# Kernel tuning notes

Hardware: AMD Instinct MI355X
Metric: run time of the kernel (lower is better)

## Reference

```python
import jax, jax.numpy as jnp
import numpy as np

B, T, D = 4, 1024, 512
H, TD = 4, 5
DH = D // H          # per-head value dim
DFF = D // 2         # Clifford FFN half-width
DR = D               # reservoir size
M = 64               # 2**mem_depth leaves
OFFSETS = (-3, -2, -1, 0)  # causal sheaf window=3
EPS = 1e-5

def _ln(x, g, b):
    m = jnp.mean(x, axis=-1, keepdims=True)
    v = jnp.mean((x - m) ** 2, axis=-1, keepdims=True)
    return (x - m) / jnp.sqrt(v + EPS) * g + b

def setup_inputs() -> dict:
    keys = iter(jax.random.split(jax.random.key(0), 64))
    def rn(shape, s=0.02):
        return (jax.random.normal(next(keys), shape) * s).astype(jnp.float32)
    x = jax.random.normal(next(keys), (B, T, D), dtype=jnp.float32)
    # sparse reservoir recurrence matrix (sparsity=0.9)
    wres_mask = (jax.random.uniform(next(keys), (DR, DR)) > 0.9).astype(jnp.float32)
    res_Wres = jax.random.normal(next(keys), (DR, DR)) * wres_mask * 0.05
    eye = jnp.eye(D, dtype=jnp.float32)
    sheaf_Rw = jnp.stack([eye + rn((D, D), 0.01) for _ in OFFSETS])  # [4,D,D]
    return dict(
        x=x,
        ln1_g=jnp.ones((D,)), ln1_b=jnp.zeros((D,)),
        ln2_g=jnp.ones((D,)), ln2_b=jnp.zeros((D,)),
        ln3_g=jnp.ones((D,)), ln3_b=jnp.zeros((D,)),
        ln4_g=jnp.ones((D,)), ln4_b=jnp.zeros((D,)),
        attn_Wp=rn((H * TD, D)), attn_bp=jnp.zeros((H * TD,)),
        attn_Wv=rn((D, D)), attn_Wo=rn((D, D)),
        ffn_Wr=rn((DFF, D)), ffn_br=jnp.zeros((DFF,)),
        ffn_Wi=rn((DFF, D)), ffn_bi=jnp.zeros((DFF,)),
        ffn_Wg=rn((D, D)), ffn_bg=jnp.zeros((D,)),
        ffn_Wout=rn((D, D)), ffn_bout=jnp.zeros((D,)),
        res_Win=rn((DR, D)), res_Wres=res_Wres,
        res_logrho=jnp.float32(0.0), res_leak=jnp.float32(0.3),
        res_readout=rn((D, DR)),
        res_v0=jax.random.normal(next(keys), (DR,), dtype=jnp.float32),
        mem_keys=rn((M, D)), mem_vals=rn((M, D)),
        mem_Wq=rn((D, D)), mem_Wout=rn((D, D)), mem_bout=jnp.zeros((D,)),
        sheaf_Rw=sheaf_Rw, sheaf_Rb=jnp.zeros((len(OFFSETS), D)),
        sheaf_alpha=jnp.float32(0.15),
    )

def reference(x, ln1_g, ln1_b, ln2_g, ln2_b, ln3_g, ln3_b, ln4_g, ln4_b,
              attn_Wp, attn_bp, attn_Wv, attn_Wo,
              ffn_Wr, ffn_br, ffn_Wi, ffn_bi, ffn_Wg, ffn_bg, ffn_Wout, ffn_bout,
              res_Win, res_Wres, res_logrho, res_leak, res_readout, res_v0,
              mem_keys, mem_vals, mem_Wq, mem_Wout, mem_bout,
              sheaf_Rw, sheaf_Rb, sheaf_alpha):
    Bx, Tx, d = x.shape

    def attn_fn(h):  # PAdicAttention, causal
        paths = jax.nn.sigmoid(h @ attn_Wp.T + attn_bp)
        paths = paths.reshape(Bx, Tx, H, TD).transpose(0, 2, 1, 3)   # [B,H,T,TD]
        pq = paths[:, :, :, None, :]
        pk = paths[:, :, None, :, :]
        agree = pq * pk + (1.0 - pq) * (1.0 - pk)                    # [B,H,T,T,TD]
        sim = jnp.sum(jnp.cumprod(agree, axis=-1), axis=-1) / TD     # [B,H,T,T]
        mask = jnp.triu(jnp.ones((Tx, Tx), bool), 1)
        sim = jnp.where(mask[None, None], -jnp.inf, sim)
        a = jax.nn.softmax(sim, axis=-1)
        V = (h @ attn_Wv.T).reshape(Bx, Tx, H, DH).transpose(0, 2, 1, 3)
        ctx = jnp.einsum('bhqk,bhkd->bhqd', a, V)
        return ctx.transpose(0, 2, 1, 3).reshape(Bx, Tx, d) @ attn_Wo.T

    def res_fn(h):  # EchoStateReservoir
        rho_t = jax.nn.sigmoid(res_logrho) * 1.5
        Wd = jax.lax.stop_gradient(res_Wres)
        def pi(v, _):
            v = Wd @ v
            n = jnp.linalg.norm(v)
            return jnp.where(n > 0, v / n, v), None
        v, _ = jax.lax.scan(pi, res_v0, None, length=3)
        rho_c = jax.lax.stop_gradient(jnp.linalg.norm(Wd @ v))
        Ws = res_Wres * (rho_t / jnp.maximum(rho_c, 1e-6))
        lk = jax.nn.sigmoid(res_leak)
        u = h @ res_Win.T                                            # [B,T,dr]
        def step(hs, ut):
            hs = (1.0 - lk) * hs + lk * jnp.tanh(hs @ Ws.T + ut)
            return hs, hs
        _, Hs = jax.lax.scan(step, jnp.zeros((Bx, DR), x.dtype), u.transpose(1, 0, 2))
        return Hs.transpose(1, 0, 2) @ res_readout.T

    def mem_fn(h):  # PAdicMemory
        q = h @ mem_Wq.T
        w = jax.nn.softmax(q @ mem_keys.T / jnp.sqrt(jnp.float32(d)), axis=-1)
        return (w @ mem_vals) @ mem_Wout.T + mem_bout

    def ffn_fn(h):  # CliffordFFN
        r = h @ ffn_Wr.T + ffn_br
        i = h @ ffn_Wi.T + ffn_bi
        prod = jnp.concatenate([r * r - i * i, 2.0 * r * i], axis=-1)
        gate = jax.nn.sigmoid(h @ ffn_Wg.T + ffn_bg)
        return (prod * gate) @ ffn_Wout.T + ffn_bout

    def sheaf_fn(h):  # SheafDiffusion, causal offsets
        lap = jnp.zeros_like(h)
        for idx, delta in enumerate(OFFSETS):
            Rx = h @ sheaf_Rw[idx].T + sheaf_Rb[idx]
            if delta == 0:
                x_nb = h
            else:
                ad = -delta
                x_nb = jnp.concatenate(
                    [jnp.zeros((Bx, ad, d), h.dtype), h[:, :Tx - ad, :]], axis=1)
            lap = lap + (Rx - x_nb) @ sheaf_Rw[idx]   # note: @ W, not W.T (as in source)
        return h - jnp.abs(sheaf_alpha) * lap

    x = x + attn_fn(_ln(x, ln1_g, ln1_b))
    x = x + res_fn(_ln(x, ln2_g, ln2_b))
    x = x + mem_fn(_ln(x, ln3_g, ln3_b))
    x = x + ffn_fn(_ln(x, ln4_g, ln4_b))
    return sheaf_fn(x)
```

## Files before the change

### kernel.cpp

```cpp
#include <hip/hip_runtime.h>
#include <hip/hip_bf16.h>
#include <stdint.h>

typedef unsigned short u16;
typedef unsigned int u32;
typedef unsigned long long u64;
typedef __bf16 bf16x8 __attribute__((ext_vector_type(8)));
typedef float f32x4 __attribute__((ext_vector_type(4)));
typedef int i32x4 __attribute__((ext_vector_type(4)));

__device__ __forceinline__ u16 f2bf(float f){
  unsigned u = __float_as_uint(f);
  u += 0x7fffu + ((u>>16)&1u);
  return (u16)(u>>16);
}
__device__ __forceinline__ float bf2f(u16 h){ return __uint_as_float((u32)h<<16); }
__device__ __forceinline__ float sigm(float x){ return 1.f/(1.f+__expf(-x)); }
__device__ __forceinline__ float tanh_fast(float x){ float e = __expf(2.f*x); return 1.f - 2.f/(e+1.f); }

__device__ __forceinline__ void gl_lds16(const void* g, void* l){
  __builtin_amdgcn_global_load_lds((const __attribute__((address_space(1))) void*)g,
                                   (__attribute__((address_space(3))) void*)l, 16, 0, 0);
}


__global__ __launch_bounds__(128) void prep_weights(
  const float* Wp, const float* Wv, const float* Wo, const float* Win, const float* rd,
  const float* Wq, const float* keys, const float* vals, const float* mWo,
  const float* Wr, const float* Wi, const float* Wg, const float* fWo, const float* Rw,
  const float* bp, const float* fbr, const float* fbi, const float* fbg,
  u16* WpB, u16* WvB, u16* WoB, u16* WinB, u16* rdB,
  u16* WqB, u16* keysB, u16* valsB, u16* mWoB,
  u16* WrB, u16* WiB, u16* WgB, u16* fWoB, u16* RwB,
  float* bpp, float* bpc, float* ss)
{
  int blk = blockIdx.x, t = threadIdx.x;
  if(blk==6912){ if(t<128) bpp[t] = (t<20)? bp[t] : 0.f; return; }
  if(blk==6913){
    for(int j=t; j<1024; j+=128)
      bpc[j] = (j<256)? fbr[j] : (j<512)? fbi[j-256] : fbg[j-512];
    return;
  }
  if(blk==6914){ if(t==0) ss[0]=1.f; else if(t<5) ss[t]=0.f; return; }
  const float* src = nullptr; u16* dst = nullptr; int r;
  bool perm = false;
  if(blk<128){ r=blk; dst=WpB+(size_t)r*512; if(r<20) src=Wp+(size_t)r*512; }
  else if(blk<640){ r=blk-128; dst=WvB+(size_t)r*512; src=Wv+(size_t)r*512; }
  else if(blk<1152){ r=blk-640; dst=WoB+(size_t)r*512; src=Wo+(size_t)r*512; }
  else if(blk<1664){ r=blk-1152; dst=WinB+(size_t)r*512; src=Win+(size_t)r*512; }
  else if(blk<2176){ r=blk-1664; dst=rdB+(size_t)r*512; src=rd+(size_t)r*512; perm=true; }
  else if(blk<2688){ r=blk-2176; dst=WqB+(size_t)r*512; src=Wq+(size_t)r*512; }
  else if(blk<2752){ r=blk-2688; dst=keysB+(size_t)r*512; src=keys+(size_t)r*512; }
  else if(blk<2816){ r=blk-2752; dst=valsB+(size_t)r*512; src=vals+(size_t)r*512; }
  else if(blk<3328){ r=blk-2816; dst=mWoB+(size_t)r*512; src=mWo+(size_t)r*512; }
  else if(blk<3584){ r=blk-3328; dst=WrB+(size_t)r*512; src=Wr+(size_t)r*512; }
  else if(blk<3840){ r=blk-3584; dst=WiB+(size_t)r*512; src=Wi+(size_t)r*512; }
  else if(blk<4352){ r=blk-3840; dst=WgB+(size_t)r*512; src=Wg+(size_t)r*512; }
  else if(blk<4864){ r=blk-4352; dst=fWoB+(size_t)r*512; src=fWo+(size_t)r*512; }
  else { r=blk-4864; dst=RwB+(size_t)r*512; src=Rw+(size_t)r*512; }
  if(src){
    float4 a = *(const float4*)&src[t*4];
    ushort4 o; o.x=f2bf(a.x); o.y=f2bf(a.y); o.z=f2bf(a.z); o.w=f2bf(a.w);
    if(perm){
      int k0 = t*4;
      int base = (k0 & ~63) | ((k0&15)<<2) | ((k0>>4)&3);
      dst[base] = o.x; dst[base+4] = o.y; dst[base+8] = o.z; dst[base+12] = o.w;
    } else {
      *(ushort4*)&dst[t*4] = o;
    }
  } else {
    ushort4 z; z.x=0; z.y=0; z.z=0; z.w=0;
    *(ushort4*)&dst[t*4] = z;
  }
}

__global__ __launch_bounds__(256) void transpose_rw(const float* __restrict__ Rw, u16* __restrict__ RwT){
  __shared__ float tl[32][33];
  int z = blockIdx.z, it = blockIdx.x, jt = blockIdx.y;
  const float* src = Rw + (size_t)z*262144;
  int r = threadIdx.x>>3, c4 = (threadIdx.x&7)*4;
  float4 v = *(const float4*)&src[(size_t)(jt*32+r)*512 + it*32 + c4];
  tl[r][c4+0]=v.x; tl[r][c4+1]=v.y; tl[r][c4+2]=v.z; tl[r][c4+3]=v.w;
  __syncthreads();
  ushort4 o;
  o.x = f2bf(tl[c4+0][r]); o.y = f2bf(tl[c4+1][r]);
  o.z = f2bf(tl[c4+2][r]); o.w = f2bf(tl[c4+3][r]);
  *(ushort4*)&RwT[(size_t)(it*32+r)*2048 + z*512 + jt*32 + c4] = o;
}

__global__ __launch_bounds__(64) void ln_kernel(const float* __restrict__ x, const float* __restrict__ g,
      const float* __restrict__ b, u16* __restrict__ out)
{
  int row = blockIdx.x, lane = threadIdx.x;
  const float* xr = x + (size_t)row*512;
  float4 v0 = *(const float4*)&xr[lane*4];
  float4 v1 = *(const float4*)&xr[256+lane*4];
  float s = v0.x+v0.y+v0.z+v0.w + v1.x+v1.y+v1.z+v1.w;
  float q = v0.x*v0.x+v0.y*v0.y+v0.z*v0.z+v0.w*v0.w + v1.x*v1.x+v1.y*v1.y+v1.z*v1.z+v1.w*v1.w;
  #pragma unroll
  for(int m=1;m<64;m<<=1){ s += __shfl_xor(s,m); q += __shfl_xor(q,m); }
  float mean = s*(1.f/512.f);
  float var  = q*(1.f/512.f) - mean*mean;
  float rstd = rsqrtf(var + 1e-5f);
  float4 g0 = *(const float4*)&g[lane*4], g1 = *(const float4*)&g[256+lane*4];
  float4 b0 = *(const float4*)&b[lane*4], b1 = *(const float4*)&b[256+lane*4];
  ushort4 o0, o1;
  o0.x = f2bf((v0.x-mean)*rstd*g0.x + b0.x); o0.y = f2bf((v0.y-mean)*rstd*g0.y + b0.y);
  o0.z = f2bf((v0.z-mean)*rstd*g0.z + b0.z); o0.w = f2bf((v0.w-mean)*rstd*g0.w + b0.w);
  o1.x = f2bf((v1.x-mean)*rstd*g1.x + b1.x); o1.y = f2bf((v1.y-mean)*rstd*g1.y + b1.y);
  o1.z = f2bf((v1.z-mean)*rstd*g1.z + b1.z); o1.w = f2bf((v1.w-mean)*rstd*g1.w + b1.w);
  *(ushort4*)&out[(size_t)row*512 + lane*4] = o0;
  *(ushort4*)&out[(size_t)row*512 + 256 + lane*4] = o1;
}

template<int EPI>
__global__ __launch_bounds__(256,2) void gemm_nt(
  const u16* __restrict__ A, const u16* __restrict__ Bw, int K, int ldc,
  float* __restrict__ outf, u16* __restrict__ outb,
  const float* __restrict__ bias, const float* __restrict__ resid,
  const float* __restrict__ aux, float* __restrict__ outf2,
  const float* __restrict__ scal, int shift_ad)
{
  __shared__ u16 Al[128*64];
  __shared__ u16 Bl[64*64];
  const int t = threadIdx.x;
  const int bm = blockIdx.x, bn = blockIdx.y;
  const int wid = t>>6, lane = t&63;
  const int wr = wid>>1, wc = wid&1;
  const int fr = lane&15, fq = lane>>4;
  f32x4 acc[4][2] = {};
  const int nK = K>>6;
  const u16* Ab = A + (size_t)(bm*128)*K;
  const u16* Bb = Bw + (size_t)(bn*64)*K;
  const int srow8 = t>>3;
  const int scol = (t&7)*8;
  char* AlB = (char*)Al; char* BlB = (char*)Bl;
  const int lbase = wid*1024;
  for(int bk=0; bk<nK; ++bk){
    #pragma unroll
    for(int c=0;c<4;++c)
      gl_lds16(&Ab[(size_t)(c*32+srow8)*K + bk*64 + scol], AlB + c*4096 + lbase);
    #pragma unroll
    for(int c=0;c<2;++c)
      gl_lds16(&Bb[(size_t)(c*32+srow8)*K + bk*64 + scol], BlB + c*4096 + lbase);
    __syncthreads();
    #pragma unroll
    for(int kk=0;kk<2;++kk){
      bf16x8 af[4], bf[2];
      #pragma unroll
      for(int m=0;m<4;++m) af[m] = *(const bf16x8*)&Al[(wr*64+m*16+fr)*64 + kk*32 + fq*8];
      #pragma unroll
      for(int n=0;n<2;++n) bf[n] = *(const bf16x8*)&Bl[(wc*32+n*16+fr)*64 + kk*32 + fq*8];
      #pragma unroll
      for(int m=0;m<4;++m)
        #pragma unroll
        for(int n=0;n<2;++n)
          acc[m][n] = __builtin_amdgcn_mfma_f32_16x16x32_bf16(af[m], bf[n], acc[m][n], 0,0,0);
    }
    __syncthreads();
  }
  float alpha = 0.f;
  if(EPI==8) alpha = fabsf(scal[0]);
  #pragma unroll
  for(int m=0;m<4;++m){
    int gr0 = bm*128 + wr*64 + m*16 + fq*4;
    #pragma unroll
    for(int n=0;n<2;++n){
      int gc = bn*64 + wc*32 + n*16 + fr;
      float bv = 0.f;
      if(EPI==2||EPI==3||EPI==5||EPI==6||EPI==9||EPI==12) bv = bias[gc];
      if(EPI==10 && gc<128) bv = bias[gc];
      #pragma unroll
      for(int i=0;i<4;++i){
        int r = gr0 + i;
        float v = acc[m][n][i] + bv;
        if(EPI==3) v = sigm(v);
        if(EPI==1||EPI==5||EPI==6) v += resid[(size_t)r*ldc + gc];
        if(EPI==8){
          outf[(size_t)r*ldc + gc] -= alpha*v;
        } else if(EPI==9){
          if(gc<512) outf[(size_t)r*512 + gc] = v;
          else       outf2[(size_t)r*512 + gc-512] = sigm(v);
        } else if(EPI==10){
          if(gc<128) outf[(size_t)r*128 + gc] = sigm(v);
          else       outf2[(size_t)r*512 + gc-128] = v;
        } else if(EPI==11){
          int pc = (gc & ~63) | ((gc&15)<<2) | ((gc>>4)&3);
          outf[(size_t)r*512 + pc] = v;
        } else if(EPI==12){
          int idx = gc>>9;
          int ad = 3 - idx;
          int ts = r & 1023;
          float xnb = 0.f;
          if(ts >= ad) xnb = bf2f(((const u16*)aux)[(size_t)(r-ad)*512 + (gc&511)]);
          outb[(size_t)r*2048 + gc] = f2bf(v - xnb);
        } else {
          if(EPI==0||EPI==1||EPI==2||EPI==3||EPI==5) outf[(size_t)r*ldc + gc] = v;
          if(EPI==6) outf2[(size_t)r*ldc + gc] = v;
          if(EPI==4||EPI==6) outb[(size_t)r*ldc + gc] = f2bf(v);
        }
      }
    }
  }
}

__global__ __launch_bounds__(128) void attn_kernel(
  const float* __restrict__ paths, const float* __restrict__ Vbuf, u16* __restrict__ ctxb)
{
  const int t = threadIdx.x;
  const int qt = blockIdx.x, bh = blockIdx.y;
  const int b = bh>>2, h = bh&3;
  const int rb = b<<10;
  const int ql = t>>2, sub = t&3;
  const int q = qt*32 + ql;
  const int wid = t>>6, lane = t&63;
  const int fr = lane&15, fq = lane>>4;
  __shared__ u16 Vl[128][72];
  __shared__ u16 Pl[32][72];
  __shared__ float pkl[64][6];
  __shared__ float scl[32];
  __shared__ float lsm[32];
  float al[5], bl[5];
  #pragma unroll
  for(int l=0;l<5;++l){
    float p = paths[(size_t)(rb+q)*128 + h*5 + l];
    al[l] = 2.f*p - 1.f; bl[l] = 1.f - p;
  }
  float m_run = -1e30f, l_run = 0.f;
  f32x4 acc[2][4] = {};
  const int nkt = (qt>>1) + 1;
  for(int kt=0; kt<nkt; ++kt){
    int k0 = kt*64;
    for(int i=t; i<320; i+=128){
      int k = i/5, l = i%5;
      pkl[k][l] = paths[(size_t)(rb+k0+k)*128 + h*5 + l];
    }
    {
      int dg = (t&31)*4, kbase = t>>5;
      #pragma unroll
      for(int i=0;i<16;++i){
        int k = kbase + i*4;
        float4 v4 = *(const float4*)&Vbuf[(size_t)(rb+k0+k)*512 + h*128 + dg];
        Vl[dg+0][k] = f2bf(v4.x); Vl[dg+1][k] = f2bf(v4.y);
        Vl[dg+2][k] = f2bf(v4.z); Vl[dg+3][k] = f2bf(v4.w);
      }
    }
    __syncthreads();
    float pj[16]; float tm = -1e30f;
    #pragma unroll
    for(int j=0;j<16;++j){
      int kidx = sub*16 + j;
      int k = k0 + kidx;
      float s;
      if(k <= q){
        float c = al[0]*pkl[kidx][0] + bl[0];
        float sa = c;
        #pragma unroll
        for(int l=1;l<5;++l){ c *= al[l]*pkl[kidx][l] + bl[l]; sa += c; }
        s = sa*0.2f;
      } else s = -1e30f;
      pj[j] = s; tm = fmaxf(tm, s);
    }
    tm = fmaxf(tm, __shfl_xor(tm,1,4));
    tm = fmaxf(tm, __shfl_xor(tm,2,4));
    float m_new = fmaxf(m_run, tm);
    float corr = __expf(m_run - m_new);
    float ls = 0.f;
    #pragma unroll
    for(int j=0;j<16;++j){
      float p = (pj[j] > -1e29f) ? __expf(pj[j]-m_new) : 0.f;
      ls += p;
      Pl[ql][sub*16+j] = f2bf(p);
    }
    l_run = l_run*corr + ls;
    m_run = m_new;
    if(sub==0) scl[ql] = corr;
    __syncthreads();
    #pragma unroll
    for(int m=0;m<2;++m){
      float c0 = scl[m*16+fq*4+0], c1 = scl[m*16+fq*4+1];
      float c2 = scl[m*16+fq*4+2], c3 = scl[m*16+fq*4+3];
      #pragma unroll
      for(int n=0;n<4;++n){ acc[m][n][0]*=c0; acc[m][n][1]*=c1; acc[m][n][2]*=c2; acc[m][n][3]*=c3; }
    }
    #pragma unroll
    for(int kk=0;kk<2;++kk){
      bf16x8 af[2], bf[4];
      #pragma unroll
      for(int m=0;m<2;++m) af[m] = *(const bf16x8*)&Pl[m*16+fr][kk*32+fq*8];
      #pragma unroll
      for(int n=0;n<4;++n) bf[n] = *(const bf16x8*)&Vl[wid*64+n*16+fr][kk*32+fq*8];
      #pragma unroll
      for(int m=0;m<2;++m)
        #pragma unroll
        for(int n=0;n<4;++n)
          acc[m][n] = __builtin_amdgcn_mfma_f32_16x16x32_bf16(af[m], bf[n], acc[m][n], 0,0,0);
    }
    __syncthreads();
  }
  {
    float lt = l_run + __shfl_xor(l_run,1,4);
    lt += __shfl_xor(lt,2,4);
    if(sub==0) lsm[ql] = lt;
  }
  __syncthreads();
  #pragma unroll
  for(int m=0;m<2;++m){
    float inv[4];
    #pragma unroll
    for(int i=0;i<4;++i) inv[i] = 1.f/lsm[m*16+fq*4+i];
    #pragma unroll
    for(int n=0;n<4;++n){
      int row = rb + qt*32 + m*16 + fq*4;
      int col = h*128 + wid*64 + n*16 + fr;
      #pragma unroll
      for(int i=0;i<4;++i)
        ctxb[(size_t)(row+i)*512 + col] = f2bf(acc[m][n][i]*inv[i]);
    }
  }
}

__global__ __launch_bounds__(256) void pmv(const float* __restrict__ W, const float* __restrict__ vin,
                    const float* __restrict__ ssin, float* __restrict__ vout, float* __restrict__ ssout)
{
  __shared__ float vs[512];
  int t = threadIdx.x;
  int j = blockIdx.x*16 + (t>>4), ks = t&15;
  float s = ssin[0];
  float inv = (s>0.f)? rsqrtf(s) : 1.f;
  vs[t] = vin[t]*inv; vs[t+256] = vin[t+256]*inv;
  __syncthreads();
  float p = 0.f;
  const float* wr = &W[(size_t)j*512 + ks*32];
  #pragma unroll
  for(int kk=0;kk<32;++kk) p += wr[kk]*vs[ks*32+kk];
  p += __shfl_xor(p,1,16); p += __shfl_xor(p,2,16); p += __shfl_xor(p,4,16); p += __shfl_xor(p,8,16);
  if(ks==0){ vout[j] = p; atomicAdd(ssout, p*p); }
}

__global__ __launch_bounds__(128) void scale_ws(const float* __restrict__ Wres, const float* __restrict__ ss4,
                         const float* __restrict__ logrho, signed char* __restrict__ WsQ,
                         float* __restrict__ wscale)
{
  __shared__ float wmax[2];
  int j = blockIdx.x, t = threadIdx.x;
  int fr = t&15, blk = t>>4;
  float rho_t = 1.5f * sigm(logrho[0]);
  float rho_c = sqrtf(ss4[0]);
  float sc = rho_t / fmaxf(rho_c, 1e-6f);
  float w[4];
  #pragma unroll
  for(int cg=0;cg<4;++cg) w[cg] = Wres[(size_t)j*512 + blk*64 + cg*16 + fr]*sc;
  float m = fmaxf(fmaxf(fabsf(w[0]),fabsf(w[1])), fmaxf(fabsf(w[2]),fabsf(w[3])));
  #pragma unroll
  for(int d=1; d<64; d<<=1) m = fmaxf(m, __shfl_xor(m, d));
  if((t&63)==0) wmax[t>>6] = m;
  __syncthreads();
  float rm = fmaxf(wmax[0], wmax[1]);
  float qs = (rm > 0.f) ? rm*(1.f/127.f) : 1.f;
  float inv = 1.f/qs;
  int q0 = __float2int_rn(w[0]*inv), q1 = __float2int_rn(w[1]*inv);
  int q2 = __float2int_rn(w[2]*inv), q3 = __float2int_rn(w[3]*inv);
  q0 = min(127,max(-127,q0)); q1 = min(127,max(-127,q1));
  q2 = min(127,max(-127,q2)); q3 = min(127,max(-127,q3));
  u32 pk = (u32)(q0&0xff) | ((u32)(q1&0xff)<<8) | ((u32)(q2&0xff)<<16) | ((u32)(q3&0xff)<<24);
  *(u32*)&WsQ[(size_t)j*512 + blk*64 + fr*4] = pk;
  if(t==0) wscale[j] = qs*(1.f/127.f);
}

__global__ __launch_bounds__(1024) void scan_kernel(
  const signed char* __restrict__ WsQ, const float* __restrict__ wscale,
  const float* __restrict__ u, const float* __restrict__ leak_p,
  u16* __restrict__ HsB)
{
  const int t = threadIdx.x;
  const int w = t>>6, lane = t&63, fr = lane&15, fq = lane>>4;
  const float lk = sigm(leak_p[0]);
  const float omlk = 1.f - lk;
  __shared__ signed char Sl[2][16*512];
  for(int i=t; i<4096; i+=1024) ((u32*)Sl)[i] = 0u;
  const int pbase = w*32 + fr*2;
  float mysc[2];
  i32x4 bw[2][8];
  #pragma unroll
  for(int cg=0; cg<2; ++cg){
    int pc = pbase + cg;
    int oc = (pc & ~63) | ((pc&3)<<4) | ((pc>>2)&15);
    mysc[cg] = wscale[oc];
    #pragma unroll
    for(int ks=0; ks<8; ++ks)
      bw[cg][ks] = *(const i32x4*)&WsQ[(size_t)oc*512 + ks*64 + fq*16];
  }
  #pragma unroll
  for(int cg=0; cg<2; ++cg)
    #pragma unroll
    for(int ks=0; ks<8; ++ks)
      asm volatile("" : "+v"(bw[cg][ks]));
  float hp0 = 0.f, hp1 = 0.f;
  const float* up = u + (size_t)(fq*1024)*512 + pbase;
  u16* hsp = HsB + (size_t)(fq*1024)*512 + pbase;
  float2 uvc = *(const float2*)up;  up += 512;
  const int rdswz = ((fr&3)<<4) ^ (((fr>>2)&3)<<6);
  const int woff = (4*fq)*512 + (pbase ^ (fq<<6));
  __syncthreads();
  for(int ts=0; ts<1024; ++ts){
    float2 uvn = *(const float2*)up;  up += 512;
    const signed char* Sb = Sl[ts&1];
    i32x4 accA[2], accB[2];
    { i32x4 z = {0,0,0,0}; accA[0]=z; accA[1]=z; accB[0]=z; accB[1]=z; }
    {
      i32x4 af[4];
      #pragma unroll
      for(int ks=0; ks<4; ++ks)
        af[ks] = *(const i32x4*)&Sb[fr*512 + ((ks*64 + fq*16) ^ rdswz)];
      #pragma unroll
      for(int ks=0; ks<4; ++ks){
        accA[0] = __builtin_amdgcn_mfma_i32_16x16x64_i8(af[ks], bw[0][ks], accA[0], 0,0,0);
        accA[1] = __builtin_amdgcn_mfma_i32_16x16x64_i8(af[ks], bw[1][ks], accA[1], 0,0,0);
      }
    }
    {
      i32x4 af[4];
      #pragma unroll
      for(int ks=0; ks<4; ++ks)
        af[ks] = *(const i32x4*)&Sb[fr*512 + (((ks+4)*64 + fq*16) ^ rdswz)];
      #pragma unroll
      for(int ks=0; ks<4; ++ks){
        accB[0] = __builtin_amdgcn_mfma_i32_16x16x64_i8(af[ks], bw[0][ks+4], accB[0], 0,0,0);
        accB[1] = __builtin_amdgcn_mfma_i32_16x16x64_i8(af[ks], bw[1][ks+4], accB[1], 0,0,0);
      }
    }
    float pre0 = (float)(accA[0][0] + accB[0][0])*mysc[0] + uvc.x;
    float pre1 = (float)(accA[1][0] + accB[1][0])*mysc[1] + uvc.y;
    float h0 = omlk*hp0 + lk*tanh_fast(pre0);
    float h1 = omlk*hp1 + lk*tanh_fast(pre1);
    hp0 = h0; hp1 = h1;
    int q0 = __float2int_rn(h0*127.f), q1 = __float2int_rn(h1*127.f);
    u16 qp = (u16)((q0&0xff) | ((q1&0xff)<<8));
    *(u16*)&Sl[(ts+1)&1][woff] = qp;
    u32 p01;
    asm volatile("v_cvt_pk_bf16_f32 %0, %1, %2" : "=v"(p01) : "v"(h0), "v"(h1));
    *(u32*)hsp = p01;  hsp += 512;
    uvc = uvn;
    asm volatile("s_waitcnt lgkmcnt(0)" ::: "memory");
    __builtin_amdgcn_s_barrier();
    asm volatile("" ::: "memory");
  }
}

__global__ __launch_bounds__(256) void mem_kernel(
  const u16* __restrict__ qb, const u16* __restrict__ keysB, const u16* __restrict__ valsB,
  u16* __restrict__ ctx2b)
{
  const int t = threadIdx.x, rt = blockIdx.x;
  const int wid = t>>6, lane = t&63, fr = lane&15, fq = lane>>4;
  __shared__ float S[64][65];
  __shared__ u16 Pl[64][72];
  __shared__ u16 VT[256][72];
  {
    f32x4 accs[4] = {};
    for(int ks=0; ks<16; ++ks){
      bf16x8 bfrag = *(const bf16x8*)&keysB[(size_t)(wid*16+fr)*512 + ks*32 + fq*8];
      #pragma unroll
      for(int mt=0;mt<4;++mt){
        bf16x8 afrag = *(const bf16x8*)&qb[(size_t)(rt*64+mt*16+fr)*512 + ks*32 + fq*8];
        accs[mt] = __builtin_amdgcn_mfma_f32_16x16x32_bf16(afrag, bfrag, accs[mt], 0,0,0);
      }
    }
    #pragma unroll
    for(int mt=0;mt<4;++mt)
      #pragma unroll
      for(int i=0;i<4;++i)
        S[mt*16+fq*4+i][wid*16+fr] = accs[mt][i];
  }
  __syncthreads();
  if(t<64){
    float m = -1e30f;
    for(int j=0;j<64;++j) m = fmaxf(m, S[t][j]);
    const float scale = 0.04419417382f;
    float sum = 0.f;
    for(int j=0;j<64;++j){ float p = __expf((S[t][j]-m)*scale); sum += p; S[t][j] = p; }
    float inv = 1.f/sum;
    for(int j=0;j<64;++j) Pl[t][j] = f2bf(S[t][j]*inv);
  }
  __syncthreads();
  for(int pass=0; pass<2; ++pass){
    {
      int k = t&63, cb = t>>6;
      #pragma unroll
      for(int i=0;i<8;++i){
        int d0 = (cb + i*4)*8;
        uint4 v = *(const uint4*)&valsB[(size_t)k*512 + pass*256 + d0];
        VT[d0+0][k]=(u16)(v.x); VT[d0+1][k]=(u16)(v.x>>16);
        VT[d0+2][k]=(u16)(v.y); VT[d0+3][k]=(u16)(v.y>>16);
        VT[d0+4][k]=(u16)(v.z); VT[d0+5][k]=(u16)(v.z>>16);
        VT[d0+6][k]=(u16)(v.w); VT[d0+7][k]=(u16)(v.w>>16);
      }
    }
    __syncthreads();
    f32x4 accp[4][4] = {};
    #pragma unroll
    for(int kk=0;kk<2;++kk){
      bf16x8 af[4], bf[4];
      #pragma unroll
      for(int mt=0;mt<4;++mt) af[mt] = *(const bf16x8*)&Pl[mt*16+fr][kk*32+fq*8];
      #pragma unroll
      for(int nt=0;nt<4;++nt) bf[nt] = *(const bf16x8*)&VT[wid*64+nt*16+fr][kk*32+fq*8];
      #pragma unroll
      for(int mt=0;mt<4;++mt)
        #pragma unroll
        for(int nt=0;nt<4;++nt)
          accp[mt][nt] = __builtin_amdgcn_mfma_f32_16x16x32_bf16(af[mt], bf[nt], accp[mt][nt], 0,0,0);
    }
    #pragma unroll
    for(int mt=0;mt<4;++mt)
      #pragma unroll
      for(int nt=0;nt<4;++nt){
        int row = rt*64 + mt*16 + fq*4;
        int col = pass*256 + wid*64 + nt*16 + fr;
        #pragma unroll
        for(int i=0;i<4;++i)
          ctx2b[(size_t)(row+i)*512 + col] = f2bf(accp[mt][nt][i]);
      }
    __syncthreads();
  }
}

__global__ __launch_bounds__(256) void prodgate(const float* __restrict__ ri, const float* __restrict__ g,
                         u16* __restrict__ pgb)
{
  int gi = blockIdx.x*256 + threadIdx.x;
  int row = gi>>7, c4 = (gi&127)*4;
  const float* base = ri + (size_t)row*512;
  float4 gv = *(const float4*)&g[(size_t)row*512 + c4];
  float4 o;
  if(c4 < 256){
    float4 r = *(const float4*)&base[c4];
    float4 ii = *(const float4*)&base[256+c4];
    o.x = (r.x*r.x - ii.x*ii.x)*gv.x; o.y = (r.y*r.y - ii.y*ii.y)*gv.y;
    o.z = (r.z*r.z - ii.z*ii.z)*gv.z; o.w = (r.w*r.w - ii.w*ii.w)*gv.w;
  } else {
    float4 r = *(const float4*)&base[c4-256];
    float4 ii = *(const float4*)&base[c4];
    o.x = 2.f*r.x*ii.x*gv.x; o.y = 2.f*r.y*ii.y*gv.y;
    o.z = 2.f*r.z*ii.z*gv.z; o.w = 2.f*r.w*ii.w*gv.w;
  }
  ushort4 us; us.x=f2bf(o.x); us.y=f2bf(o.y); us.z=f2bf(o.z); us.w=f2bf(o.w);
  *(ushort4*)&pgb[(size_t)row*512 + c4] = us;
}

static void launch_gemm(int epi, dim3 grid, const u16* A, const u16* B, int K, int ldc,
  float* outf, u16* outb, const float* bias, const float* resid, const float* aux,
  float* outf2, const float* scal, int ad, hipStream_t s)
{
  switch(epi){
    case 0: gemm_nt<0><<<grid,256,0,s>>>(A,B,K,ldc,outf,outb,bias,resid,aux,outf2,scal,ad); break;
    case 1: gemm_nt<1><<<grid,256,0,s>>>(A,B,K,ldc,outf,outb,bias,resid,aux,outf2,scal,ad); break;
    case 4: gemm_nt<4><<<grid,256,0,s>>>(A,B,K,ldc,outf,outb,bias,resid,aux,outf2,scal,ad); break;
    case 5: gemm_nt<5><<<grid,256,0,s>>>(A,B,K,ldc,outf,outb,bias,resid,aux,outf2,scal,ad); break;
    case 6: gemm_nt<6><<<grid,256,0,s>>>(A,B,K,ldc,outf,outb,bias,resid,aux,outf2,scal,ad); break;
    case 8: gemm_nt<8><<<grid,256,0,s>>>(A,B,K,ldc,outf,outb,bias,resid,aux,outf2,scal,ad); break;
    case 9: gemm_nt<9><<<grid,256,0,s>>>(A,B,K,ldc,outf,outb,bias,resid,aux,outf2,scal,ad); break;
    case 10: gemm_nt<10><<<grid,256,0,s>>>(A,B,K,ldc,outf,outb,bias,resid,aux,outf2,scal,ad); break;
    case 11: gemm_nt<11><<<grid,256,0,s>>>(A,B,K,ldc,outf,outb,bias,resid,aux,outf2,scal,ad); break;
    case 12: gemm_nt<12><<<grid,256,0,s>>>(A,B,K,ldc,outf,outb,bias,resid,aux,outf2,scal,ad); break;
  }
}

extern "C" void kernel_launch(void* const* d_in, const int* in_sizes, int n_in,
                              void* d_out, int out_size, void* d_ws, size_t ws_size,
                              hipStream_t stream)
{
  const float* x      = (const float*)d_in[0];
  const float* ln1g   = (const float*)d_in[1];  const float* ln1b = (const float*)d_in[2];
  const float* ln2g   = (const float*)d_in[3];  const float* ln2b = (const float*)d_in[4];
  const float* ln3g   = (const float*)d_in[5];  const float* ln3b = (const float*)d_in[6];
  const float* ln4g   = (const float*)d_in[7];  const float* ln4b = (const float*)d_in[8];
  const float* aWp    = (const float*)d_in[9];  const float* abp  = (const float*)d_in[10];
  const float* aWv    = (const float*)d_in[11]; const float* aWo  = (const float*)d_in[12];
  const float* fWr    = (const float*)d_in[13]; const float* fbr  = (const float*)d_in[14];
  const float* fWi    = (const float*)d_in[15]; const float* fbi  = (const float*)d_in[16];
  const float* fWg    = (const float*)d_in[17]; const float* fbg  = (const float*)d_in[18];
  const float* fWo    = (const float*)d_in[19]; const float* fbo  = (const float*)d_in[20];
  const float* rWin   = (const float*)d_in[21]; const float* rWres= (const float*)d_in[22];
  const float* rlogr  = (const float*)d_in[23]; const float* rleak= (const float*)d_in[24];
  const float* rread  = (const float*)d_in[25]; const float* rv0  = (const float*)d_in[26];
  const float* mkeys  = (const float*)d_in[27]; const float* mvals= (const float*)d_in[28];
  const float* mWq    = (const float*)d_in[29]; const float* mWo  = (const float*)d_in[30];
  const float* mbo    = (const float*)d_in[31];
  const float* sRw    = (const float*)d_in[32]; const float* sRb  = (const float*)d_in[33];
  const float* salpha = (const float*)d_in[34];
  (void)in_sizes; (void)n_in; (void)out_size;

  char* ws = (char*)d_ws;
  float* XCUR  = (float*)(ws + 0);
  u16*   X4B   = (u16*)  (ws + 8388608);
  u16*   HB    = (u16*)  (ws + 8388608);
  float* VU    = (float*)(ws + 12582912);
  u16*   TBUF  = (u16*)  (ws + 12582912);
  float* PATHS = (float*)(ws + 20971520);
  u16*   CTXB  = (u16*)  (ws + 23068672);
  u16*   HSB   = (u16*)  (ws + 27262976);
  char* WB = ws + 31457280;
  u16* WpB   = (u16*)(WB + 0);
  u16* WvB   = (u16*)(WB + 131072);
  u16* WoB   = (u16*)(WB + 655360);
  u16* WinB  = (u16*)(WB + 1179648);
  u16* rdB   = (u16*)(WB + 1703936);
  u16* WqB   = (u16*)(WB + 2228224);
  u16* keysB = (u16*)(WB + 2752512);
  u16* valsB = (u16*)(WB + 2818048);
  u16* mWoB  = (u16*)(WB + 2883584);
  u16* WrB   = (u16*)(WB + 3407872);
  u16* WiB   = (u16*)(WB + 3670016);
  u16* WgB   = (u16*)(WB + 3932160);
  u16* fWoB  = (u16*)(WB + 4456448);
  u16* RwB   = (u16*)(WB + 4980736);
  u16* RwTB  = (u16*)(WB + 7077888);
  signed char* WsQ = (signed char*)(WB + 9175040);
  float* wscale = (float*)(WB + 9437184);
  float* bpp = (float*)(WB + 9699328);
  float* bpc = (float*)(WB + 9699840);
  float* ssv = (float*)(WB + 9733632);
  float* vr  = (float*)(WB + 9733696);
  float* GATE = (float*)d_out;

  if(ws_size < (size_t)41200000) return;

  prep_weights<<<6915,128,0,stream>>>(aWp,aWv,aWo,rWin,rread,mWq,mkeys,mvals,mWo,fWr,fWi,fWg,fWo,sRw,
      abp, fbr, fbi, fbg,
      WpB,WvB,WoB,WinB,rdB,WqB,keysB,valsB,mWoB,WrB,WiB,WgB,fWoB,RwB,bpp,bpc,ssv);
  transpose_rw<<<dim3(16,16,4),256,0,stream>>>(sRw, RwTB);

  dim3 g512(32,8), g640(32,10), g1024(32,16), g2048(32,32);

  ln_kernel<<<4096,64,0,stream>>>(x, ln1g, ln1b, HB);
  launch_gemm(10, g640, HB, WpB, 512, 0, PATHS, nullptr, bpp, nullptr, nullptr, VU, nullptr, 0, stream);
  attn_kernel<<<dim3(32,16),128,0,stream>>>(PATHS, VU, CTXB);
  launch_gemm(1, g512, CTXB, WoB, 512, 512, XCUR, nullptr, nullptr, x, nullptr, nullptr, nullptr, 0, stream);

  ln_kernel<<<4096,64,0,stream>>>(XCUR, ln2g, ln2b, HB);
  launch_gemm(11, g512, HB, WinB, 512, 512, VU, nullptr, nullptr, nullptr, nullptr, nullptr, nullptr, 0, stream);
  pmv<<<32,256,0,stream>>>(rWres, rv0,   &ssv[0], &vr[0],    &ssv[1]);
  pmv<<<32,256,0,stream>>>(rWres, &vr[0],   &ssv[1], &vr[512],  &ssv[2]);
  pmv<<<32,256,0,stream>>>(rWres, &vr[512], &ssv[2], &vr[1024], &ssv[3]);
  pmv<<<32,256,0,stream>>>(rWres, &vr[1024],&ssv[3], &vr[1536], &ssv[4]);
  scale_ws<<<512,128,0,stream>>>(rWres, &ssv[4], rlogr, WsQ, wscale);
  scan_kernel<<<1,1024,0,stream>>>(WsQ, wscale, VU, rleak, HSB);
  launch_gemm(1, g512, HSB, rdB, 512, 512, XCUR, nullptr, nullptr, XCUR, nullptr, nullptr, nullptr, 0, stream);

  ln_kernel<<<4096,64,0,stream>>>(XCUR, ln3g, ln3b, HB);
  launch_gemm(4, g512, HB, WqB, 512, 512, nullptr, CTXB, nullptr, nullptr, nullptr, nullptr, nullptr, 0, stream);
  mem_kernel<<<64,256,0,stream>>>(CTXB, keysB, valsB, HSB);
  launch_gemm(5, g512, HSB, mWoB, 512, 512, XCUR, nullptr, mbo, XCUR, nullptr, nullptr, nullptr, 0, stream);

  ln_kernel<<<4096,64,0,stream>>>(XCUR, ln4g, ln4b, HB);
  launch_gemm(9, g1024, HB, WrB, 512, 0, VU, nullptr, bpc, nullptr, nullptr, GATE, nullptr, 0, stream);
  prodgate<<<2048,256,0,stream>>>(VU, GATE, CTXB);
  launch_gemm(6, g512, CTXB, fWoB, 512, 512, nullptr, X4B, fbo, XCUR, nullptr, (float*)d_out, nullptr, 0, stream);

  launch_gemm(12, g2048, X4B, RwB, 512, 0, nullptr, TBUF, sRb, nullptr, (const float*)X4B, nullptr, nullptr, 0, stream);
  launch_gemm(8, g512, TBUF, RwTB, 2048, 512, (float*)d_out, nullptr, nullptr, nullptr, nullptr, nullptr, salpha, 0, stream);
}
```

Measured before the change: 1.167 ms.

## Double-buffer GEMM LDS tiles and defer reservoir state stores off the critical path

The GEMM mainloop now uses two LDS buffers. It prefetches the next K-tile via global_load_lds while computing MFMAs on the current one, which replaces the load-then-sync pattern with a single wait and barrier per iteration. The reservoir recurrence delays each step's bf16 hidden-state global store to the next iteration, so the store no longer sits right before the barrier. The unused EPI 2/3 epilogue branches are removed. LDS use per block doubles, which may lower occupancy under launch_bounds(256,2).

```diff
diff --git a/kernel.cpp b/kernel.cpp
--- a/kernel.cpp
+++ b/kernel.cpp
@@ -121,8 +121,8 @@
   const float* __restrict__ aux, float* __restrict__ outf2,
   const float* __restrict__ scal, int shift_ad)
 {
-  __shared__ u16 Al[128*64];
-  __shared__ u16 Bl[64*64];
+  __shared__ u16 Al[2][128*64];
+  __shared__ u16 Bl[2][64*64];
   const int t = threadIdx.x;
   const int bm = blockIdx.x, bn = blockIdx.y;
   const int wid = t>>6, lane = t&63;
@@ -136,28 +136,43 @@
   const int scol = (t&7)*8;
   char* AlB = (char*)Al; char* BlB = (char*)Bl;
   const int lbase = wid*1024;
+  #pragma unroll
+  for(int c=0;c<4;++c)
+    gl_lds16(&Ab[(size_t)(c*32+srow8)*K + scol], AlB + c*4096 + lbase);
+  #pragma unroll
+  for(int c=0;c<2;++c)
+    gl_lds16(&Bb[(size_t)(c*32+srow8)*K + scol], BlB + c*4096 + lbase);
+  asm volatile("s_waitcnt vmcnt(0)" ::: "memory");
+  __builtin_amdgcn_s_barrier();
+  asm volatile("" ::: "memory");
   for(int bk=0; bk<nK; ++bk){
-    #pragma unroll
-    for(int c=0;c<4;++c)
-      gl_lds16(&Ab[(size_t)(c*32+srow8)*K + bk*64 + scol], AlB + c*4096 + lbase);
-    #pragma unroll
-    for(int c=0;c<2;++c)
-      gl_lds16(&Bb[(size_t)(c*32+srow8)*K + bk*64 + scol], BlB + c*4096 + lbase);
-    __syncthreads();
+    const int cur = bk&1, nxt = cur^1;
+    if(bk+1 < nK){
+      #pragma unroll
+      for(int c=0;c<4;++c)
+        gl_lds16(&Ab[(size_t)(c*32+srow8)*K + (bk+1)*64 + scol], AlB + nxt*16384 + c*4096 + lbase);
+      #pragma unroll
+      for(int c=0;c<2;++c)
+        gl_lds16(&Bb[(size_t)(c*32+srow8)*K + (bk+1)*64 + scol], BlB + nxt*8192 + c*4096 + lbase);
+    }
+    const u16* Ac = Al[cur];
+    const u16* Bc = Bl[cur];
     #pragma unroll
     for(int kk=0;kk<2;++kk){
       bf16x8 af[4], bf[2];
       #pragma unroll
-      for(int m=0;m<4;++m) af[m] = *(const bf16x8*)&Al[(wr*64+m*16+fr)*64 + kk*32 + fq*8];
-      #pragma unroll
-      for(int n=0;n<2;++n) bf[n] = *(const bf16x8*)&Bl[(wc*32+n*16+fr)*64 + kk*32 + fq*8];
+      for(int m=0;m<4;++m) af[m] = *(const bf16x8*)&Ac[(wr*64+m*16+fr)*64 + kk*32 + fq*8];
+      #pragma unroll
+      for(int n=0;n<2;++n) bf[n] = *(const bf16x8*)&Bc[(wc*32+n*16+fr)*64 + kk*32 + fq*8];
       #pragma unroll
       for(int m=0;m<4;++m)
         #pragma unroll
         for(int n=0;n<2;++n)
           acc[m][n] = __builtin_amdgcn_mfma_f32_16x16x32_bf16(af[m], bf[n], acc[m][n], 0,0,0);
     }
-    __syncthreads();
+    asm volatile("s_waitcnt vmcnt(0)" ::: "memory");
+    __builtin_amdgcn_s_barrier();
+    asm volatile("" ::: "memory");
   }
   float alpha = 0.f;
   if(EPI==8) alpha = fabsf(scal[0]);
@@ -168,13 +183,12 @@
     for(int n=0;n<2;++n){
       int gc = bn*64 + wc*32 + n*16 + fr;
       float bv = 0.f;
-      if(EPI==2||EPI==3||EPI==5||EPI==6||EPI==9||EPI==12) bv = bias[gc];
+      if(EPI==5||EPI==6||EPI==9||EPI==12) bv = bias[gc];
       if(EPI==10 && gc<128) bv = bias[gc];
       #pragma unroll
       for(int i=0;i<4;++i){
         int r = gr0 + i;
         float v = acc[m][n][i] + bv;
-        if(EPI==3) v = sigm(v);
         if(EPI==1||EPI==5||EPI==6) v += resid[(size_t)r*ldc + gc];
         if(EPI==8){
           outf[(size_t)r*ldc + gc] -= alpha*v;
@@ -195,7 +209,7 @@
           if(ts >= ad) xnb = bf2f(((const u16*)aux)[(size_t)(r-ad)*512 + (gc&511)]);
           outb[(size_t)r*2048 + gc] = f2bf(v - xnb);
         } else {
-          if(EPI==0||EPI==1||EPI==2||EPI==3||EPI==5) outf[(size_t)r*ldc + gc] = v;
+          if(EPI==0||EPI==1||EPI==5) outf[(size_t)r*ldc + gc] = v;
           if(EPI==6) outf2[(size_t)r*ldc + gc] = v;
           if(EPI==4||EPI==6) outb[(size_t)r*ldc + gc] = f2bf(v);
         }
@@ -402,9 +416,11 @@
   float2 uvc = *(const float2*)up;  up += 512;
   const int rdswz = ((fr&3)<<4) ^ (((fr>>2)&3)<<6);
   const int woff = (4*fq)*512 + (pbase ^ (fq<<6));
+  u32 p01v = 0u;
   __syncthreads();
   for(int ts=0; ts<1024; ++ts){
     float2 uvn = *(const float2*)up;  up += 512;
+    if(ts > 0){ *(u32*)hsp = p01v;  hsp += 512; }
     const signed char* Sb = Sl[ts&1];
     i32x4 accA[2], accB[2];
     { i32x4 z = {0,0,0,0}; accA[0]=z; accA[1]=z; accB[0]=z; accB[1]=z; }
@@ -438,14 +454,13 @@
     int q0 = __float2int_rn(h0*127.f), q1 = __float2int_rn(h1*127.f);
     u16 qp = (u16)((q0&0xff) | ((q1&0xff)<<8));
     *(u16*)&Sl[(ts+1)&1][woff] = qp;
-    u32 p01;
-    asm volatile("v_cvt_pk_bf16_f32 %0, %1, %2" : "=v"(p01) : "v"(h0), "v"(h1));
-    *(u32*)hsp = p01;  hsp += 512;
+    asm volatile("v_cvt_pk_bf16_f32 %0, %1, %2" : "=v"(p01v) : "v"(h0), "v"(h1));
     uvc = uvn;
     asm volatile("s_waitcnt lgkmcnt(0)" ::: "memory");
     __builtin_amdgcn_s_barrier();
     asm volatile("" ::: "memory");
   }
+  *(u32*)hsp = p01v;
 }
 
 __global__ __launch_bounds__(256) void mem_kernel(
```

New measurement: 1.170 ms. Within noise of the previous version (+0.2%).
